# Kernel optimization log

Hardware: AMD Instinct MI355X
Metric: run time of the kernel (lower is better)

The kernel has to match this reference:

```python
import jax, jax.numpy as jnp
import numpy as np

BN_EPS = 1e-5
GRID_W = 17  # conv output width hardcoded via lat_idx*17+lon_idx

def _conv(x, w, b, stride):
    y = jax.lax.conv_general_dilated(x, w, (stride, stride), [(1, 1), (1, 1)],
                                     dimension_numbers=("NCHW", "OIHW", "NCHW"))
    return y + b[None, :, None, None]

def _bn_eval(x, g, b):
    # running_mean=0, running_var=1 (fresh BatchNorm in eval mode)
    inv = jnp.float32(1.0 / np.sqrt(1.0 + BN_EPS))
    return x * (g[None, :, None, None] * inv) + b[None, :, None, None]

def setup_inputs() -> dict:
    key = jax.random.key(0)
    ks = iter(jax.random.split(key, 64))
    def rn(shape, s=0.05):
        return jax.random.normal(next(ks), shape, jnp.float32) * s
    B, S, K = 512, 128, 64
    NR = 100000
    inp = {}
    inp["roads"] = jax.random.randint(next(ks), (B, S), 0, NR)
    inp["ratios"] = jax.random.uniform(next(ks), (B, S), jnp.float32) * 0.9 + 0.1
    inp["T"] = jax.random.normal(next(ks), (1, 1, 138, 138), jnp.float32)
    inp["lon_idx"] = jax.random.randint(next(ks), (B, K), 0, 17)
    inp["lat_idx"] = jax.random.randint(next(ks), (B, K), 0, 17)
    inp["lengths"] = jax.random.uniform(next(ks), (NR,), jnp.float32) * 100.0 + 1.0
    inp["map_u"] = jnp.arange(NR, dtype=jnp.int32)
    inp["map_s1"] = jax.random.randint(next(ks), (NR,), 0, 14)
    inp["map_s2"] = jax.random.randint(next(ks), (NR,), 0, 7)
    inp["map_s3"] = jax.random.randint(next(ks), (NR,), 0, 2)
    inp["emb_u"] = rn((NR, 128))
    inp["emb_s1"] = rn((14, 16)); inp["emb_s2"] = rn((7, 8)); inp["emb_s3"] = rn((2, 4))
    inp["rho_w1"] = rn((156, 512)); inp["rho_b1"] = jnp.zeros((512,), jnp.float32)
    inp["rho_w21"] = rn((512, 128)); inp["rho_b21"] = jnp.zeros((128,), jnp.float32)
    inp["conv1_w"] = rn((32, 1, 5, 5)); inp["conv1_b"] = jnp.zeros((32,), jnp.float32)
    inp["bn1_g"] = jnp.ones((32,), jnp.float32); inp["bn1_b"] = jnp.zeros((32,), jnp.float32)
    inp["conv2_w"] = rn((64, 32, 4, 4)); inp["conv2_b"] = jnp.zeros((64,), jnp.float32)
    inp["bn2_g"] = jnp.ones((64,), jnp.float32); inp["bn2_b"] = jnp.zeros((64,), jnp.float32)
    inp["conv3_w"] = rn((128, 64, 4, 4)); inp["conv3_b"] = jnp.zeros((128,), jnp.float32)
    inp["bn3_g"] = jnp.ones((128,), jnp.float32); inp["bn3_b"] = jnp.zeros((128,), jnp.float32)
    inp["f2_w1"] = rn((128, 256)); inp["f2_b1"] = jnp.zeros((256,), jnp.float32)
    inp["f2_w2"] = rn((256, 128)); inp["f2_b2"] = jnp.zeros((128,), jnp.float32)
    inp["f_w1"] = rn((256, 512)); inp["f_b1"] = jnp.zeros((512,), jnp.float32)
    inp["f_w21"] = rn((512, 1)); inp["f_b21"] = jnp.zeros((1,), jnp.float32)
    inp["f_w22"] = rn((512, 1)); inp["f_b22"] = jnp.zeros((1,), jnp.float32)
    return inp

def reference(roads, ratios, T, lon_idx, lat_idx, lengths, map_u, map_s1, map_s2, map_s3,
              emb_u, emb_s1, emb_s2, emb_s3, rho_w1, rho_b1, rho_w21, rho_b21,
              conv1_w, conv1_b, bn1_g, bn1_b, conv2_w, conv2_b, bn2_g, bn2_b,
              conv3_w, conv3_b, bn3_g, bn3_b, f2_w1, f2_b1, f2_w2, f2_b2,
              f_w1, f_b1, f_w21, f_b21, f_w22, f_b22):
    # road lengths / weights
    road_lens = lengths[roads] * ratios               # (B,S)
    l = road_lens.sum(axis=1)                         # (B,)
    w = road_lens / l[:, None]                        # (B,S)
    # ProbRho (eval: dropout=id, reparameterize -> mu)
    u = emb_u[map_u[roads]]                           # (B,S,128)
    s1 = emb_s1[map_s1[roads]]; s2 = emb_s2[map_s2[roads]]; s3 = emb_s3[map_s3[roads]]
    x = jnp.concatenate([u, s1, s2, s3], axis=2)      # (B,S,156)
    h = jax.nn.relu(x @ rho_w1 + rho_b1)
    rho = h @ rho_w21 + rho_b21                       # (B,S,128)
    # ProbTraffic_spatial conv stack
    t = jax.nn.leaky_relu(_bn_eval(_conv(T, conv1_w, conv1_b, 2), bn1_g, bn1_b), 0.1)
    t = jax.nn.leaky_relu(_bn_eval(_conv(t, conv2_w, conv2_b, 2), bn2_g, bn2_b), 0.1)
    t = jax.nn.leaky_relu(_bn_eval(_conv(t, conv3_w, conv3_b, 2), bn3_g, bn3_b), 0.1)  # (1,128,17,17)
    c_flat = jnp.transpose(t[0], (1, 2, 0)).reshape(-1, t.shape[1])  # (289,128)
    # fused segment gather + mean over each trajectory's grid cells
    idx = lat_idx * GRID_W + lon_idx                  # (B,K)
    c_mean = c_flat[idx].mean(axis=1)                 # (B,128)
    h2 = jax.nn.selu(c_mean @ f2_w1 + f2_b1)
    c2 = h2 @ f2_w2 + f2_b2                           # (B,128)
    # ProbTravelTime
    xcat = jnp.concatenate([rho, jnp.broadcast_to(c2[:, None, :], rho.shape)], axis=2)  # (B,S,256)
    h3 = jax.nn.relu(xcat @ f_w1 + f_b1)              # (B,S,512)
    logm = (h3 @ f_w21 + f_b21)[..., 0]               # (B,S)
    logv = (h3 @ f_w22 + f_b22)[..., 0]
    logw = jnp.log(w)
    logm_agg = jax.nn.logsumexp(logm + logw, axis=1)
    logv_agg = jax.nn.logsumexp(logv + 2.0 * logw, axis=1)
    logl = jnp.log(l)
    logmu = logl - logm_agg
    loglam = logl - 3.0 * logm_agg - logv_agg
    return (logmu, loglam)
```

## Files before the change

kernel.cpp:

```cpp
#include <hip/hip_runtime.h>
#include <math.h>

#define BB 512
#define SS 128
#define NROWS (BB*SS)
#define TMG 64
#define NBLKG (NROWS/TMG)

__device__ __forceinline__ float leaky01(float x){ return x >= 0.f ? x : 0.1f*x; }

#define BN_INV 0.9999950000374997f
#define SELU_A 1.6732632423543772f
#define SELU_S 1.0507009873554805f

typedef __attribute__((ext_vector_type(8))) short short8;
typedef __attribute__((ext_vector_type(4))) float f32x4;

__device__ __forceinline__ unsigned short f2bf(float f) {
    unsigned int u = __float_as_uint(f);
    u += 0x7fff + ((u >> 16) & 1);
    return (unsigned short)(u >> 16);
}
__device__ __forceinline__ uint2 pack4bf(float a, float b, float c, float d) {
    uint2 r;
    r.x = (unsigned int)f2bf(a) | ((unsigned int)f2bf(b) << 16);
    r.y = (unsigned int)f2bf(c) | ((unsigned int)f2bf(d) << 16);
    return r;
}

__device__ __forceinline__ unsigned short* h1p(unsigned short* base, int row, int col) {
    unsigned off = (unsigned)(row*1024 + col*2);
    off ^= (unsigned)((row & 7) << 4);
    return (unsigned short*)((char*)base + off);
}

#define PREP_N (278528 + 32768 + 131072)
#define PREP_BLOCKS (PREP_N/256)
#define CONV1_BLOCKS 578

__global__ __launch_bounds__(256) void combo1_kernel(
    const float* __restrict__ w1, const float* __restrict__ w21, const float* __restrict__ fw1,
    unsigned short* __restrict__ sw1, unsigned short* __restrict__ sw21, unsigned short* __restrict__ sw3,
    const float* __restrict__ c2w_in, const float* __restrict__ c3w_in,
    float* __restrict__ w2t, float* __restrict__ w3t,
    const float* __restrict__ T, const float* __restrict__ cw,
    const float* __restrict__ cbias, const float* __restrict__ g,
    const float* __restrict__ bb, float* __restrict__ out)
{
    if (blockIdx.x < PREP_BLOCKS) {
        int t = blockIdx.x*256 + threadIdx.x;
        if (t < 81920) {
            int j = t & 7; int r = t >> 3; int lane = r & 63; r >>= 6;
            int ks = r % 5; int nt = r / 5;
            int n = nt*16 + (lane & 15);
            int k = ks*32 + (lane >> 4)*8 + j;
            float v = (k < 156) ? w1[k*512 + n] : 0.f;
            sw1[t] = f2bf(v);
        } else if (t < 147456) {
            int u = t - 81920;
            int j = u & 7; int r = u >> 3; int lane = r & 63; r >>= 6;
            int ks = r & 15; int nt = r >> 4;
            int d = nt*16 + (lane & 15);
            int k = ks*32 + (lane >> 4)*8 + j;
            sw21[u] = f2bf(w21[k*128 + d]);
        } else if (t < 278528) {
            int u = t - 147456;
            int j = u & 7; int r = u >> 3; int lane = r & 63; r >>= 6;
            int ks = r & 7; int nt = r >> 3;
            int n = nt*16 + (lane & 15);
            int k = ks*32 + (lane >> 4)*8 + j;
            sw3[u] = f2bf(fw1[k*512 + n]);
        } else if (t < 278528 + 32768) {
            int u = t - 278528;
            int oc = u >> 9; int r = u & 511;
            int kk = r >> 5; int ic = r & 31;
            w2t[u] = c2w_in[oc*512 + ic*16 + kk];
        } else {
            int u = t - (278528 + 32768);
            int oc = u >> 10; int r = u & 1023;
            int kk = r >> 6; int ic = r & 63;
            w3t[u] = c3w_in[oc*1024 + ic*16 + kk];
        }
    } else {
        int t = (blockIdx.x - PREP_BLOCKS)*256 + threadIdx.x;
        if (t >= 32*68*68) return;
        int oc  = t & 31;
        int pos = t >> 5;
        int oy = pos / 68, ox = pos % 68;
        float acc = cbias[oc];
        #pragma unroll
        for (int ky=0; ky<5; ++ky) {
            int iy = oy*2 - 1 + ky;
            if (iy < 0 || iy >= 138) continue;
            #pragma unroll
            for (int kx=0; kx<5; ++kx) {
                int ix = ox*2 - 1 + kx;
                if (ix < 0 || ix >= 138) continue;
                acc += cw[oc*25 + ky*5 + kx] * T[iy*138 + ix];
            }
        }
        acc = acc * (g[oc]*BN_INV) + bb[oc];
        out[pos*32 + oc] = leaky01(acc);
    }
}

__global__ __launch_bounds__(256) void conv2_kernel(
    const float* __restrict__ in,
    const float* __restrict__ w2t,
    const float* __restrict__ bias, const float* __restrict__ g,
    const float* __restrict__ bb, float* __restrict__ out)
{
    int gid = blockIdx.x*256 + threadIdx.x;
    if (gid >= 64*34*34*4) return;
    int icg = gid & 3;
    int o   = gid >> 2;
    int oc  = o & 63;
    int pos = o >> 6;
    int oy = pos / 34, ox = pos % 34;
    float acc = 0.f;
    #pragma unroll
    for (int ky=0; ky<4; ++ky) {
        int iy = oy*2 - 1 + ky;
        if (iy < 0 || iy >= 68) continue;
        #pragma unroll
        for (int kx=0; kx<4; ++kx) {
            int ix = ox*2 - 1 + kx;
            if (ix < 0 || ix >= 68) continue;
            const float* ip = &in[(iy*68+ix)*32 + icg*8];
            const float* wp = &w2t[oc*512 + (ky*4+kx)*32 + icg*8];
            float4 i0 = *(const float4*)ip, i1 = *(const float4*)(ip+4);
            float4 w0 = *(const float4*)wp, w1v = *(const float4*)(wp+4);
            acc += i0.x*w0.x + i0.y*w0.y + i0.z*w0.z + i0.w*w0.w
                 + i1.x*w1v.x + i1.y*w1v.y + i1.z*w1v.z + i1.w*w1v.w;
        }
    }
    acc += __shfl_xor(acc, 1, 64);
    acc += __shfl_xor(acc, 2, 64);
    if (icg == 0) {
        acc = (acc + bias[oc]) * (g[oc]*BN_INV) + bb[oc];
        out[pos*64 + oc] = leaky01(acc);
    }
}

__global__ __launch_bounds__(256) void conv3_kernel(
    const float* __restrict__ in,
    const float* __restrict__ w3t,
    const float* __restrict__ bias, const float* __restrict__ g,
    const float* __restrict__ bb, float* __restrict__ outT)
{
    int gid = blockIdx.x*256 + threadIdx.x;
    if (gid >= 128*289*8) return;
    int icg = gid & 7;
    int o   = gid >> 3;
    int oc  = o & 127;
    int pos = o >> 7;
    int oy = pos / 17, ox = pos % 17;
    float acc = 0.f;
    #pragma unroll
    for (int ky=0; ky<4; ++ky) {
        int iy = oy*2 - 1 + ky;
        if (iy < 0 || iy >= 34) continue;
        #pragma unroll
        for (int kx=0; kx<4; ++kx) {
            int ix = ox*2 - 1 + kx;
            if (ix < 0 || ix >= 34) continue;
            const float* ip = &in[(iy*34+ix)*64 + icg*8];
            const float* wp = &w3t[oc*1024 + (ky*4+kx)*64 + icg*8];
            float4 i0 = *(const float4*)ip, i1 = *(const float4*)(ip+4);
            float4 w0 = *(const float4*)wp, w1v = *(const float4*)(wp+4);
            acc += i0.x*w0.x + i0.y*w0.y + i0.z*w0.z + i0.w*w0.w
                 + i1.x*w1v.x + i1.y*w1v.y + i1.z*w1v.z + i1.w*w1v.w;
        }
    }
    acc += __shfl_xor(acc, 1, 64);
    acc += __shfl_xor(acc, 2, 64);
    acc += __shfl_xor(acc, 4, 64);
    if (icg == 0) {
        acc = (acc + bias[oc]) * (g[oc]*BN_INV) + bb[oc];
        outT[pos*128 + oc] = leaky01(acc);
    }
}

__global__ __launch_bounds__(256) void cmh2c2_kernel(
    const float* __restrict__ t3T, const int* __restrict__ lat, const int* __restrict__ lon,
    const float* __restrict__ w1, const float* __restrict__ b1,
    const float* __restrict__ w2, const float* __restrict__ b2,
    float* __restrict__ c2b)
{
    __shared__ int   ps[64];
    __shared__ float part[256];
    __shared__ float cms[128];
    __shared__ float h2s[256];
    const int b = blockIdx.x;
    const int tid = threadIdx.x;
    if (tid < 64) ps[tid] = lat[b*64+tid]*17 + lon[b*64+tid];
    __syncthreads();
    {
        int d = tid & 127, half = tid >> 7;
        float s = 0.f;
        #pragma unroll 8
        for (int k=0; k<32; ++k) s += t3T[ps[half*32+k]*128 + d];
        part[tid] = s;
    }
    __syncthreads();
    if (tid < 128) cms[tid] = (part[tid] + part[tid+128]) * (1.f/64.f);
    __syncthreads();
    {
        float acc = b1[tid];
        #pragma unroll 8
        for (int k=0; k<128; ++k) acc += cms[k] * w1[k*256 + tid];
        h2s[tid] = acc > 0.f ? SELU_S*acc : SELU_S*SELU_A*(expf(acc)-1.f);
    }
    __syncthreads();
    {
        int d = tid & 127, half = tid >> 7;
        float acc = 0.f;
        #pragma unroll 8
        for (int k=0; k<128; ++k) acc += h2s[half*128 + k] * w2[(half*128+k)*128 + d];
        part[tid] = acc;
    }
    __syncthreads();
    if (tid < 128) c2b[b*128 + tid] = part[tid] + part[tid+128] + b2[tid];
}

#define XS_S 168
#define XC_S 264

__global__ __launch_bounds__(512, 4) void mega_kernel(
    const int* __restrict__ roads,
    const int* __restrict__ map_u, const int* __restrict__ map_s1,
    const int* __restrict__ map_s2, const int* __restrict__ map_s3,
    const float* __restrict__ emb_u, const float* __restrict__ emb_s1,
    const float* __restrict__ emb_s2, const float* __restrict__ emb_s3,
    const unsigned short* __restrict__ sw1, const float* __restrict__ b1,
    const unsigned short* __restrict__ sw21, const float* __restrict__ b21,
    const float* __restrict__ c2,
    const unsigned short* __restrict__ sw3, const float* __restrict__ fb1,
    const float* __restrict__ fw21, const float* __restrict__ fb21,
    const float* __restrict__ fw22, const float* __restrict__ fb22,
    float* __restrict__ logm, float* __restrict__ logv)
{
    __shared__ unsigned short buf[32768];
    unsigned short* xs  = buf;
    unsigned short* xcs = buf;
    float* pmv = (float*)buf;

    const int tid  = threadIdx.x;
    const int wid  = tid >> 6;
    const int lane = tid & 63;
    const int lo   = lane & 15;
    const int hi   = lane >> 4;
    const int r0   = blockIdx.x * TMG;
    const int b    = r0 >> 7;

    short8 afp[4];
    #pragma unroll
    for (int mt=0;mt<4;++mt)
        afp[mt] = *(const short8*)&sw1[((wid*4+mt)*5 + 0)*512 + lane*8];

    {
        int row = tid >> 3, seg = tid & 7;
        int road = roads[r0 + row];
        const float* src = emb_u + (long)map_u[road]*128 + seg*16;
        #pragma unroll
        for (int i=0;i<4;++i) {
            float4 v = *(const float4*)&src[i*4];
            *(uint2*)&xs[row*XS_S + seg*16 + i*4] = pack4bf(v.x, v.y, v.z, v.w);
        }
    }
    for (int idx = tid; idx < 64*32; idx += 512) {
        int row = idx >> 5, k2 = idx & 31;
        int road = roads[r0 + row];
        float v;
        if      (k2 < 16) v = emb_s1[map_s1[road]*16 + k2];
        else if (k2 < 24) v = emb_s2[map_s2[road]*8  + (k2-16)];
        else if (k2 < 28) v = emb_s3[map_s3[road]*4  + (k2-24)];
        else              v = 0.f;
        xs[row*XS_S + 128 + k2] = f2bf(v);
    }
    __syncthreads();

    short8 a2p;
    f32x4 acc1[4][4];
    {
        #pragma unroll
        for (int mt=0;mt<4;++mt)
            #pragma unroll
            for (int rg=0;rg<4;++rg) acc1[mt][rg]=(f32x4)(0.f);
        #pragma unroll
        for (int ks=0; ks<5; ++ks) {
            const int kb = ks*32 + hi*8;
            short8 bf[4];
            #pragma unroll
            for (int rg=0;rg<4;++rg)
                bf[rg] = *(const short8*)&xs[(rg*16+lo)*XS_S + kb];
            short8 af[4];
            if (ks == 0) {
                #pragma unroll
                for (int mt=0;mt<4;++mt) af[mt] = afp[mt];
            } else {
                #pragma unroll
                for (int mt=0;mt<4;++mt)
                    af[mt] = *(const short8*)&sw1[((wid*4+mt)*5 + ks)*512 + lane*8];
            }
            #pragma unroll
            for (int mt=0;mt<4;++mt)
                #pragma unroll
                for (int rg=0;rg<4;++rg)
                    acc1[mt][rg] = __builtin_amdgcn_mfma_f32_16x16x32_bf16(af[mt], bf[rg], acc1[mt][rg], 0,0,0);
        }
    }
    __syncthreads();

    {
        a2p = *(const short8*)&sw21[(wid*16 + 0)*512 + lane*8];
        const int n0 = wid * 64;
        #pragma unroll
        for (int mt=0;mt<4;++mt) {
            const int nb = n0 + mt*16 + hi*4;
            float4 bias = *(const float4*)&b1[nb];
            const float* bp = (const float*)&bias;
            #pragma unroll
            for (int rg=0;rg<4;++rg) {
                const float* a = (const float*)&acc1[mt][rg];
                float y0 = fmaxf(a[0]+bp[0], 0.f), y1 = fmaxf(a[1]+bp[1], 0.f);
                float y2 = fmaxf(a[2]+bp[2], 0.f), y3 = fmaxf(a[3]+bp[3], 0.f);
                *(uint2*)h1p(buf, rg*16+lo, nb) = pack4bf(y0,y1,y2,y3);
            }
        }
    }
    __syncthreads();

    short8 a3p[4];
    f32x4 acc2[4];
    {
        #pragma unroll
        for (int rg=0;rg<4;++rg) acc2[rg]=(f32x4)(0.f);
        #pragma unroll 4
        for (int ks=0; ks<16; ++ks) {
            const int kb = ks*32 + hi*8;
            short8 bf[4];
            #pragma unroll
            for (int rg=0;rg<4;++rg)
                bf[rg] = *(const short8*)h1p(buf, rg*16+lo, kb);
            short8 a = (ks == 0) ? a2p
                     : *(const short8*)&sw21[(wid*16 + ks)*512 + lane*8];
            #pragma unroll
            for (int rg=0;rg<4;++rg)
                acc2[rg] = __builtin_amdgcn_mfma_f32_16x16x32_bf16(a, bf[rg], acc2[rg], 0,0,0);
        }
    }
    __syncthreads();

    {
        #pragma unroll
        for (int mt=0;mt<4;++mt)
            a3p[mt] = *(const short8*)&sw3[((wid*4+mt)*8 + 0)*512 + lane*8];
        const int nb = wid*16 + hi*4;
        float4 bias = *(const float4*)&b21[nb];
        const float* bp = (const float*)&bias;
        #pragma unroll
        for (int rg=0;rg<4;++rg) {
            const float* a = (const float*)&acc2[rg];
            *(uint2*)&xcs[(rg*16+lo)*XC_S + nb] =
                pack4bf(a[0]+bp[0], a[1]+bp[1], a[2]+bp[2], a[3]+bp[3]);
        }
        int row = tid >> 3, seg = tid & 7;
        const float* src = c2 + b*128 + seg*16;
        #pragma unroll
        for (int i=0;i<4;++i) {
            float4 v = *(const float4*)&src[i*4];
            *(uint2*)&xcs[row*XC_S + 128 + seg*16 + i*4] = pack4bf(v.x, v.y, v.z, v.w);
        }
    }
    __syncthreads();

    {
        const int n0 = wid * 64;
        f32x4 acc[4][4];
        #pragma unroll
        for (int mt=0;mt<4;++mt)
            #pragma unroll
            for (int rg=0;rg<4;++rg) acc[mt][rg]=(f32x4)(0.f);
        #pragma unroll 2
        for (int ks=0; ks<8; ++ks) {
            const int kb = ks*32 + hi*8;
            short8 bf[4];
            #pragma unroll
            for (int rg=0;rg<4;++rg)
                bf[rg] = *(const short8*)&xcs[(rg*16+lo)*XC_S + kb];
            short8 af[4];
            if (ks == 0) {
                #pragma unroll
                for (int mt=0;mt<4;++mt) af[mt] = a3p[mt];
            } else {
                #pragma unroll
                for (int mt=0;mt<4;++mt)
                    af[mt] = *(const short8*)&sw3[((wid*4+mt)*8 + ks)*512 + lane*8];
            }
            #pragma unroll
            for (int mt=0;mt<4;++mt)
                #pragma unroll
                for (int rg=0;rg<4;++rg)
                    acc[mt][rg] = __builtin_amdgcn_mfma_f32_16x16x32_bf16(af[mt], bf[rg], acc[mt][rg], 0,0,0);
        }
        float sm[4] = {0.f,0.f,0.f,0.f};
        float sv[4] = {0.f,0.f,0.f,0.f};
        #pragma unroll
        for (int mt=0;mt<4;++mt) {
            const int nb = n0 + mt*16 + hi*4;
            float4 bias = *(const float4*)&fb1[nb];
            float4 wm   = *(const float4*)&fw21[nb];
            float4 wv   = *(const float4*)&fw22[nb];
            const float *bp=(const float*)&bias, *wmp=(const float*)&wm, *wvp=(const float*)&wv;
            #pragma unroll
            for (int rg=0;rg<4;++rg) {
                const float* a = (const float*)&acc[mt][rg];
                #pragma unroll
                for (int j=0;j<4;++j) {
                    float y = fmaxf(a[j]+bp[j], 0.f);
                    sm[rg] += y*wmp[j];
                    sv[rg] += y*wvp[j];
                }
            }
        }
        #pragma unroll
        for (int rg=0;rg<4;++rg) {
            sm[rg] += __shfl_xor(sm[rg], 16, 64); sm[rg] += __shfl_xor(sm[rg], 32, 64);
            sv[rg] += __shfl_xor(sv[rg], 16, 64); sv[rg] += __shfl_xor(sv[rg], 32, 64);
        }
        __syncthreads();
        if (hi == 0) {
            #pragma unroll
            for (int rg=0;rg<4;++rg) {
                pmv[wid*64 + rg*16 + lo]       = sm[rg];
                pmv[512 + wid*64 + rg*16 + lo] = sv[rg];
            }
        }
    }
    __syncthreads();
    if (tid < 64) {
        float sm = 0.f, sv = 0.f;
        #pragma unroll
        for (int w=0; w<8; ++w) {
            sm += pmv[w*64 + tid];
            sv += pmv[512 + w*64 + tid];
        }
        logm[r0+tid] = sm + fb21[0];
        logv[r0+tid] = sv + fb22[0];
    }
}

__global__ __launch_bounds__(64) void final_kernel(
    const int* __restrict__ roads, const float* __restrict__ ratios,
    const float* __restrict__ lengths,
    const float* __restrict__ logm, const float* __restrict__ logv,
    float* __restrict__ out)
{
    int b = blockIdx.x;
    int lane = threadIdx.x;
    int i0 = b*128 + lane;
    int i1 = i0 + 64;
    float rl0 = lengths[roads[i0]] * ratios[i0];
    float rl1 = lengths[roads[i1]] * ratios[i1];

    float tsum = rl0 + rl1;
    #pragma unroll
    for (int off=32; off; off>>=1) tsum += __shfl_xor(tsum, off, 64);
    float l = tsum;
    float logl = logf(l);

    float lw0 = logf(rl0) - logl;
    float lw1 = logf(rl1) - logl;

    float am0 = logm[i0] + lw0, am1 = logm[i1] + lw1;
    float av0 = logv[i0] + 2.f*lw0, av1 = logv[i1] + 2.f*lw1;

    float mm = fmaxf(am0, am1);
    #pragma unroll
    for (int off=32; off; off>>=1) mm = fmaxf(mm, __shfl_xor(mm, off, 64));
    float se = expf(am0-mm) + expf(am1-mm);
    #pragma unroll
    for (int off=32; off; off>>=1) se += __shfl_xor(se, off, 64);
    float lsem = logf(se) + mm;

    float mv = fmaxf(av0, av1);
    #pragma unroll
    for (int off=32; off; off>>=1) mv = fmaxf(mv, __shfl_xor(mv, off, 64));
    float sev = expf(av0-mv) + expf(av1-mv);
    #pragma unroll
    for (int off=32; off; off>>=1) sev += __shfl_xor(sev, off, 64);
    float lsev = logf(sev) + mv;

    if (lane == 0) {
        out[b]       = logl - lsem;
        out[512 + b] = logl - 3.f*lsem - lsev;
    }
}

extern "C" void kernel_launch(void* const* d_in, const int* in_sizes, int n_in,
                              void* d_out, int out_size, void* d_ws, size_t ws_size,
                              hipStream_t stream) {
    const int*   roads   = (const int*)  d_in[0];
    const float* ratios  = (const float*)d_in[1];
    const float* T       = (const float*)d_in[2];
    const int*   lon_idx = (const int*)  d_in[3];
    const int*   lat_idx = (const int*)  d_in[4];
    const float* lengths = (const float*)d_in[5];
    const int*   map_u   = (const int*)  d_in[6];
    const int*   map_s1  = (const int*)  d_in[7];
    const int*   map_s2  = (const int*)  d_in[8];
    const int*   map_s3  = (const int*)  d_in[9];
    const float* emb_u   = (const float*)d_in[10];
    const float* emb_s1  = (const float*)d_in[11];
    const float* emb_s2  = (const float*)d_in[12];
    const float* emb_s3  = (const float*)d_in[13];
    const float* rho_w1  = (const float*)d_in[14];
    const float* rho_b1  = (const float*)d_in[15];
    const float* rho_w21 = (const float*)d_in[16];
    const float* rho_b21 = (const float*)d_in[17];
    const float* conv1_w = (const float*)d_in[18];
    const float* conv1_b = (const float*)d_in[19];
    const float* bn1_g   = (const float*)d_in[20];
    const float* bn1_b   = (const float*)d_in[21];
    const float* conv2_w = (const float*)d_in[22];
    const float* conv2_b = (const float*)d_in[23];
    const float* bn2_g   = (const float*)d_in[24];
    const float* bn2_b   = (const float*)d_in[25];
    const float* conv3_w = (const float*)d_in[26];
    const float* conv3_b = (const float*)d_in[27];
    const float* bn3_g   = (const float*)d_in[28];
    const float* bn3_b   = (const float*)d_in[29];
    const float* f2_w1   = (const float*)d_in[30];
    const float* f2_b1   = (const float*)d_in[31];
    const float* f2_w2   = (const float*)d_in[32];
    const float* f2_b2   = (const float*)d_in[33];
    const float* f_w1    = (const float*)d_in[34];
    const float* f_b1    = (const float*)d_in[35];
    const float* f_w21   = (const float*)d_in[36];
    const float* f_b21   = (const float*)d_in[37];
    const float* f_w22   = (const float*)d_in[38];
    const float* f_b22   = (const float*)d_in[39];

    float* ws    = (float*)d_ws;
    float* t1    = ws;
    float* t2    = t1 + 147968;
    float* t3T   = t2 + 73984;
    float* c2b   = t3T + 36992;
    float* logm  = c2b + 65536;
    float* logv  = logm + 65536;
    float* w2t   = logv + 65536;
    float* w3t   = w2t + 32768;
    unsigned short* sw1  = (unsigned short*)(w3t + 131072);
    unsigned short* sw21 = sw1 + 81920;
    unsigned short* sw3  = sw21 + 65536;

    combo1_kernel<<<PREP_BLOCKS + CONV1_BLOCKS, 256, 0, stream>>>(
        rho_w1, rho_w21, f_w1, sw1, sw21, sw3,
        conv2_w, conv3_w, w2t, w3t,
        T, conv1_w, conv1_b, bn1_g, bn1_b, t1);
    conv2_kernel<<<(64*34*34*4 + 255)/256, 256, 0, stream>>>(t1, w2t, conv2_b, bn2_g, bn2_b, t2);
    conv3_kernel<<<(128*289*8 + 255)/256, 256, 0, stream>>>(t2, w3t, conv3_b, bn3_g, bn3_b, t3T);
    cmh2c2_kernel<<<512, 256, 0, stream>>>(t3T, lat_idx, lon_idx, f2_w1, f2_b1, f2_w2, f2_b2, c2b);
    mega_kernel<<<NBLKG, 512, 0, stream>>>(roads, map_u, map_s1, map_s2, map_s3,
                                           emb_u, emb_s1, emb_s2, emb_s3,
                                           sw1, rho_b1, sw21, rho_b21,
                                           c2b, sw3, f_b1, f_w21, f_b21, f_w22, f_b22,
                                           logm, logv);
    final_kernel<<<512, 64, 0, stream>>>(roads, ratios, lengths, logm, logv, (float*)d_out);
}
```

Baseline: 117.6 us.

## Process whole trajectory per block and fuse final logsumexp into mega kernel

The MLP mega kernel now handles all 128 rows of one trajectory per block with 1024 threads and 128 KB of shared memory, instead of 64 rows per block with 512 threads. Because each block owns a full trajectory, the weighted logsumexp reduction from the separate final kernel is folded in. This removes the logm/logv global round trip and one kernel launch. The warp-to-tile mapping changes so each warp covers fewer output columns over more rows, and new XOR-swizzled shared layouts replace the padded strides. The trade-off is higher register and shared-memory pressure per block, which can lower occupancy with only 512 blocks.

Measured after the change: 117.2 us. Within noise of the previous version (-0.3%).

```diff
diff --git a/kernel.cpp b/kernel.cpp
--- a/kernel.cpp
+++ b/kernel.cpp
@@ -4,7 +4,7 @@
 #define BB 512
 #define SS 128
 #define NROWS (BB*SS)
-#define TMG 64
+#define TMG 128
 #define NBLKG (NROWS/TMG)
 
 __device__ __forceinline__ float leaky01(float x){ return x >= 0.f ? x : 0.1f*x; }
@@ -28,8 +28,18 @@
     return r;
 }
 
+__device__ __forceinline__ unsigned short* xsp(unsigned short* base, int row, int col) {
+    unsigned off = (unsigned)(row*384 + col*2);
+    off ^= (unsigned)((row & 7) << 4);
+    return (unsigned short*)((char*)base + off);
+}
 __device__ __forceinline__ unsigned short* h1p(unsigned short* base, int row, int col) {
     unsigned off = (unsigned)(row*1024 + col*2);
+    off ^= (unsigned)((row & 7) << 4);
+    return (unsigned short*)((char*)base + off);
+}
+__device__ __forceinline__ unsigned short* xcp(unsigned short* base, int row, int col) {
+    unsigned off = (unsigned)(row*512 + col*2);
     off ^= (unsigned)((row & 7) << 4);
     return (unsigned short*)((char*)base + off);
 }
@@ -223,11 +233,9 @@
     if (tid < 128) c2b[b*128 + tid] = part[tid] + part[tid+128] + b2[tid];
 }
 
-#define XS_S 168
-#define XC_S 264
-
-__global__ __launch_bounds__(512, 4) void mega_kernel(
-    const int* __restrict__ roads,
+__global__ __launch_bounds__(1024, 4) void mega_kernel(
+    const int* __restrict__ roads, const float* __restrict__ ratios,
+    const float* __restrict__ lengths,
     const int* __restrict__ map_u, const int* __restrict__ map_s1,
     const int* __restrict__ map_s2, const int* __restrict__ map_s3,
     const float* __restrict__ emb_u, const float* __restrict__ emb_s1,
@@ -238,25 +246,24 @@
     const unsigned short* __restrict__ sw3, const float* __restrict__ fb1,
     const float* __restrict__ fw21, const float* __restrict__ fb21,
     const float* __restrict__ fw22, const float* __restrict__ fb22,
-    float* __restrict__ logm, float* __restrict__ logv)
+    float* __restrict__ out)
 {
-    __shared__ unsigned short buf[32768];
-    unsigned short* xs  = buf;
-    unsigned short* xcs = buf;
+    __shared__ unsigned short buf[65536];
     float* pmv = (float*)buf;
+    float* fin = (float*)buf + 4096;
 
     const int tid  = threadIdx.x;
     const int wid  = tid >> 6;
     const int lane = tid & 63;
     const int lo   = lane & 15;
     const int hi   = lane >> 4;
-    const int r0   = blockIdx.x * TMG;
-    const int b    = r0 >> 7;
-
-    short8 afp[4];
+    const int b    = blockIdx.x;
+    const int r0   = b * TMG;
+
+    short8 afp[2];
     #pragma unroll
-    for (int mt=0;mt<4;++mt)
-        afp[mt] = *(const short8*)&sw1[((wid*4+mt)*5 + 0)*512 + lane*8];
+    for (int mt=0;mt<2;++mt)
+        afp[mt] = *(const short8*)&sw1[((wid*2+mt)*5 + 0)*512 + lane*8];
 
     {
         int row = tid >> 3, seg = tid & 7;
@@ -265,10 +272,10 @@
         #pragma unroll
         for (int i=0;i<4;++i) {
             float4 v = *(const float4*)&src[i*4];
-            *(uint2*)&xs[row*XS_S + seg*16 + i*4] = pack4bf(v.x, v.y, v.z, v.w);
-        }
-    }
-    for (int idx = tid; idx < 64*32; idx += 512) {
+            *(uint2*)xsp(buf, row, seg*16 + i*4) = pack4bf(v.x, v.y, v.z, v.w);
+        }
+    }
+    for (int idx = tid; idx < 128*32; idx += 1024) {
         int row = idx >> 5, k2 = idx & 31;
         int road = roads[r0 + row];
         float v;
@@ -276,52 +283,47 @@
         else if (k2 < 24) v = emb_s2[map_s2[road]*8  + (k2-16)];
         else if (k2 < 28) v = emb_s3[map_s3[road]*4  + (k2-24)];
         else              v = 0.f;
-        xs[row*XS_S + 128 + k2] = f2bf(v);
+        *xsp(buf, row, 128 + k2) = f2bf(v);
     }
     __syncthreads();
 
     short8 a2p;
-    f32x4 acc1[4][4];
-    {
-        #pragma unroll
-        for (int mt=0;mt<4;++mt)
-            #pragma unroll
-            for (int rg=0;rg<4;++rg) acc1[mt][rg]=(f32x4)(0.f);
+    f32x4 acc1[2][8];
+    {
+        #pragma unroll
+        for (int mt=0;mt<2;++mt)
+            #pragma unroll
+            for (int rg=0;rg<8;++rg) acc1[mt][rg]=(f32x4)(0.f);
         #pragma unroll
         for (int ks=0; ks<5; ++ks) {
             const int kb = ks*32 + hi*8;
-            short8 bf[4];
-            #pragma unroll
-            for (int rg=0;rg<4;++rg)
-                bf[rg] = *(const short8*)&xs[(rg*16+lo)*XS_S + kb];
-            short8 af[4];
-            if (ks == 0) {
+            short8 af[2];
+            if (ks == 0) { af[0]=afp[0]; af[1]=afp[1]; }
+            else {
                 #pragma unroll
-                for (int mt=0;mt<4;++mt) af[mt] = afp[mt];
-            } else {
-                #pragma unroll
-                for (int mt=0;mt<4;++mt)
-                    af[mt] = *(const short8*)&sw1[((wid*4+mt)*5 + ks)*512 + lane*8];
-            }
-            #pragma unroll
-            for (int mt=0;mt<4;++mt)
-                #pragma unroll
-                for (int rg=0;rg<4;++rg)
-                    acc1[mt][rg] = __builtin_amdgcn_mfma_f32_16x16x32_bf16(af[mt], bf[rg], acc1[mt][rg], 0,0,0);
-        }
-    }
-    __syncthreads();
-
-    {
-        a2p = *(const short8*)&sw21[(wid*16 + 0)*512 + lane*8];
-        const int n0 = wid * 64;
-        #pragma unroll
-        for (int mt=0;mt<4;++mt) {
+                for (int mt=0;mt<2;++mt)
+                    af[mt] = *(const short8*)&sw1[((wid*2+mt)*5 + ks)*512 + lane*8];
+            }
+            #pragma unroll
+            for (int rg=0;rg<8;++rg) {
+                short8 bf = *(const short8*)xsp(buf, rg*16+lo, kb);
+                acc1[0][rg] = __builtin_amdgcn_mfma_f32_16x16x32_bf16(af[0], bf, acc1[0][rg], 0,0,0);
+                acc1[1][rg] = __builtin_amdgcn_mfma_f32_16x16x32_bf16(af[1], bf, acc1[1][rg], 0,0,0);
+            }
+        }
+    }
+    __syncthreads();
+
+    {
+        a2p = *(const short8*)&sw21[((wid>>1)*16 + 0)*512 + lane*8];
+        const int n0 = wid * 32;
+        #pragma unroll
+        for (int mt=0;mt<2;++mt) {
             const int nb = n0 + mt*16 + hi*4;
             float4 bias = *(const float4*)&b1[nb];
             const float* bp = (const float*)&bias;
             #pragma unroll
-            for (int rg=0;rg<4;++rg) {
+            for (int rg=0;rg<8;++rg) {
                 const float* a = (const float*)&acc1[mt][rg];
                 float y0 = fmaxf(a[0]+bp[0], 0.f), y1 = fmaxf(a[1]+bp[1], 0.f);
                 float y2 = fmaxf(a[2]+bp[2], 0.f), y3 = fmaxf(a[3]+bp[3], 0.f);
@@ -331,38 +333,38 @@
     }
     __syncthreads();
 
-    short8 a3p[4];
+    short8 a3p[2];
     f32x4 acc2[4];
-    {
-        #pragma unroll
-        for (int rg=0;rg<4;++rg) acc2[rg]=(f32x4)(0.f);
+    const int nt2 = wid >> 1;
+    const int rh  = wid & 1;
+    {
+        #pragma unroll
+        for (int i=0;i<4;++i) acc2[i]=(f32x4)(0.f);
         #pragma unroll 4
         for (int ks=0; ks<16; ++ks) {
             const int kb = ks*32 + hi*8;
-            short8 bf[4];
-            #pragma unroll
-            for (int rg=0;rg<4;++rg)
-                bf[rg] = *(const short8*)h1p(buf, rg*16+lo, kb);
             short8 a = (ks == 0) ? a2p
-                     : *(const short8*)&sw21[(wid*16 + ks)*512 + lane*8];
-            #pragma unroll
-            for (int rg=0;rg<4;++rg)
-                acc2[rg] = __builtin_amdgcn_mfma_f32_16x16x32_bf16(a, bf[rg], acc2[rg], 0,0,0);
-        }
-    }
-    __syncthreads();
-
-    {
-        #pragma unroll
-        for (int mt=0;mt<4;++mt)
-            a3p[mt] = *(const short8*)&sw3[((wid*4+mt)*8 + 0)*512 + lane*8];
-        const int nb = wid*16 + hi*4;
+                     : *(const short8*)&sw21[(nt2*16 + ks)*512 + lane*8];
+            #pragma unroll
+            for (int i=0;i<4;++i) {
+                short8 bf = *(const short8*)h1p(buf, (rh*4+i)*16+lo, kb);
+                acc2[i] = __builtin_amdgcn_mfma_f32_16x16x32_bf16(a, bf, acc2[i], 0,0,0);
+            }
+        }
+    }
+    __syncthreads();
+
+    {
+        #pragma unroll
+        for (int mt=0;mt<2;++mt)
+            a3p[mt] = *(const short8*)&sw3[((wid*2+mt)*8 + 0)*512 + lane*8];
+        const int nb = nt2*16 + hi*4;
         float4 bias = *(const float4*)&b21[nb];
         const float* bp = (const float*)&bias;
         #pragma unroll
-        for (int rg=0;rg<4;++rg) {
-            const float* a = (const float*)&acc2[rg];
-            *(uint2*)&xcs[(rg*16+lo)*XC_S + nb] =
+        for (int i=0;i<4;++i) {
+            const float* a = (const float*)&acc2[i];
+            *(uint2*)xcp(buf, (rh*4+i)*16+lo, nb) =
                 pack4bf(a[0]+bp[0], a[1]+bp[1], a[2]+bp[2], a[3]+bp[3]);
         }
         int row = tid >> 3, seg = tid & 7;
@@ -370,51 +372,47 @@
         #pragma unroll
         for (int i=0;i<4;++i) {
             float4 v = *(const float4*)&src[i*4];
-            *(uint2*)&xcs[row*XC_S + 128 + seg*16 + i*4] = pack4bf(v.x, v.y, v.z, v.w);
-        }
-    }
-    __syncthreads();
-
-    {
-        const int n0 = wid * 64;
-        f32x4 acc[4][4];
-        #pragma unroll
-        for (int mt=0;mt<4;++mt)
-            #pragma unroll
-            for (int rg=0;rg<4;++rg) acc[mt][rg]=(f32x4)(0.f);
+            *(uint2*)xcp(buf, row, 128 + seg*16 + i*4) = pack4bf(v.x, v.y, v.z, v.w);
+        }
+    }
+    __syncthreads();
+
+    float sm[8], sv[8];
+    {
+        const int n0 = wid * 32;
+        f32x4 acc[2][8];
+        #pragma unroll
+        for (int mt=0;mt<2;++mt)
+            #pragma unroll
+            for (int rg=0;rg<8;++rg) acc[mt][rg]=(f32x4)(0.f);
         #pragma unroll 2
         for (int ks=0; ks<8; ++ks) {
             const int kb = ks*32 + hi*8;
-            short8 bf[4];
-            #pragma unroll
-            for (int rg=0;rg<4;++rg)
-                bf[rg] = *(const short8*)&xcs[(rg*16+lo)*XC_S + kb];
-            short8 af[4];
-            if (ks == 0) {
+            short8 af[2];
+            if (ks == 0) { af[0]=a3p[0]; af[1]=a3p[1]; }
+            else {
                 #pragma unroll
-                for (int mt=0;mt<4;++mt) af[mt] = a3p[mt];
-            } else {
-                #pragma unroll
-                for (int mt=0;mt<4;++mt)
-                    af[mt] = *(const short8*)&sw3[((wid*4+mt)*8 + ks)*512 + lane*8];
-            }
-            #pragma unroll
-            for (int mt=0;mt<4;++mt)
-                #pragma unroll
-                for (int rg=0;rg<4;++rg)
-                    acc[mt][rg] = __builtin_amdgcn_mfma_f32_16x16x32_bf16(af[mt], bf[rg], acc[mt][rg], 0,0,0);
-        }
-        float sm[4] = {0.f,0.f,0.f,0.f};
-        float sv[4] = {0.f,0.f,0.f,0.f};
-        #pragma unroll
-        for (int mt=0;mt<4;++mt) {
+                for (int mt=0;mt<2;++mt)
+                    af[mt] = *(const short8*)&sw3[((wid*2+mt)*8 + ks)*512 + lane*8];
+            }
+            #pragma unroll
+            for (int rg=0;rg<8;++rg) {
+                short8 bf = *(const short8*)xcp(buf, rg*16+lo, kb);
+                acc[0][rg] = __builtin_amdgcn_mfma_f32_16x16x32_bf16(af[0], bf, acc[0][rg], 0,0,0);
+                acc[1][rg] = __builtin_amdgcn_mfma_f32_16x16x32_bf16(af[1], bf, acc[1][rg], 0,0,0);
+            }
+        }
+        #pragma unroll
+        for (int rg=0;rg<8;++rg){ sm[rg]=0.f; sv[rg]=0.f; }
+        #pragma unroll
+        for (int mt=0;mt<2;++mt) {
             const int nb = n0 + mt*16 + hi*4;
             float4 bias = *(const float4*)&fb1[nb];
             float4 wm   = *(const float4*)&fw21[nb];
             float4 wv   = *(const float4*)&fw22[nb];
             const float *bp=(const float*)&bias, *wmp=(const float*)&wm, *wvp=(const float*)&wv;
             #pragma unroll
-            for (int rg=0;rg<4;++rg) {
+            for (int rg=0;rg<8;++rg) {
                 const float* a = (const float*)&acc[mt][rg];
                 #pragma unroll
                 for (int j=0;j<4;++j) {
@@ -425,74 +423,66 @@
             }
         }
         #pragma unroll
-        for (int rg=0;rg<4;++rg) {
+        for (int rg=0;rg<8;++rg) {
             sm[rg] += __shfl_xor(sm[rg], 16, 64); sm[rg] += __shfl_xor(sm[rg], 32, 64);
             sv[rg] += __shfl_xor(sv[rg], 16, 64); sv[rg] += __shfl_xor(sv[rg], 32, 64);
         }
-        __syncthreads();
-        if (hi == 0) {
-            #pragma unroll
-            for (int rg=0;rg<4;++rg) {
-                pmv[wid*64 + rg*16 + lo]       = sm[rg];
-                pmv[512 + wid*64 + rg*16 + lo] = sv[rg];
-            }
-        }
-    }
-    __syncthreads();
-    if (tid < 64) {
-        float sm = 0.f, sv = 0.f;
-        #pragma unroll
-        for (int w=0; w<8; ++w) {
-            sm += pmv[w*64 + tid];
-            sv += pmv[512 + w*64 + tid];
-        }
-        logm[r0+tid] = sm + fb21[0];
-        logv[r0+tid] = sv + fb22[0];
-    }
-}
-
-__global__ __launch_bounds__(64) void final_kernel(
-    const int* __restrict__ roads, const float* __restrict__ ratios,
-    const float* __restrict__ lengths,
-    const float* __restrict__ logm, const float* __restrict__ logv,
-    float* __restrict__ out)
-{
-    int b = blockIdx.x;
-    int lane = threadIdx.x;
-    int i0 = b*128 + lane;
-    int i1 = i0 + 64;
-    float rl0 = lengths[roads[i0]] * ratios[i0];
-    float rl1 = lengths[roads[i1]] * ratios[i1];
-
-    float tsum = rl0 + rl1;
-    #pragma unroll
-    for (int off=32; off; off>>=1) tsum += __shfl_xor(tsum, off, 64);
-    float l = tsum;
-    float logl = logf(l);
-
-    float lw0 = logf(rl0) - logl;
-    float lw1 = logf(rl1) - logl;
-
-    float am0 = logm[i0] + lw0, am1 = logm[i1] + lw1;
-    float av0 = logv[i0] + 2.f*lw0, av1 = logv[i1] + 2.f*lw1;
-
-    float mm = fmaxf(am0, am1);
-    #pragma unroll
-    for (int off=32; off; off>>=1) mm = fmaxf(mm, __shfl_xor(mm, off, 64));
-    float se = expf(am0-mm) + expf(am1-mm);
-    #pragma unroll
-    for (int off=32; off; off>>=1) se += __shfl_xor(se, off, 64);
-    float lsem = logf(se) + mm;
-
-    float mv = fmaxf(av0, av1);
-    #pragma unroll
-    for (int off=32; off; off>>=1) mv = fmaxf(mv, __shfl_xor(mv, off, 64));
-    float sev = expf(av0-mv) + expf(av1-mv);
-    #pragma unroll
-    for (int off=32; off; off>>=1) sev += __shfl_xor(sev, off, 64);
-    float lsev = logf(sev) + mv;
-
-    if (lane == 0) {
+    }
+    __syncthreads();
+    if (hi == 0) {
+        #pragma unroll
+        for (int rg=0;rg<8;++rg) {
+            pmv[wid*128 + rg*16 + lo]        = sm[rg];
+            pmv[2048 + wid*128 + rg*16 + lo] = sv[rg];
+        }
+    }
+    __syncthreads();
+
+    float rl = 0.f, am = 0.f, av = 0.f;
+    if (tid < 128) {
+        float s_m = 0.f, s_v = 0.f;
+        #pragma unroll
+        for (int w=0; w<16; ++w) {
+            s_m += pmv[w*128 + tid];
+            s_v += pmv[2048 + w*128 + tid];
+        }
+        s_m += fb21[0]; s_v += fb22[0];
+        int gi = r0 + tid;
+        rl = lengths[roads[gi]] * ratios[gi];
+        float ws = rl;
+        #pragma unroll
+        for (int off=32; off; off>>=1) ws += __shfl_xor(ws, off, 64);
+        if (lane == 0) fin[wid] = ws;
+        am = s_m; av = s_v;
+    }
+    __syncthreads();
+    if (tid < 128) {
+        float l = fin[0] + fin[1];
+        float logl = logf(l);
+        float lw = logf(rl) - logl;
+        am += lw; av += 2.f*lw;
+        fin[16] = logl;
+        float mm = am, mv = av;
+        #pragma unroll
+        for (int off=32; off; off>>=1) { mm = fmaxf(mm, __shfl_xor(mm, off, 64)); mv = fmaxf(mv, __shfl_xor(mv, off, 64)); }
+        if (lane == 0) { fin[2+wid] = mm; fin[4+wid] = mv; fin[8+wid] = logl; }
+    }
+    __syncthreads();
+    if (tid < 128) {
+        float mm = fmaxf(fin[2], fin[3]);
+        float mv = fmaxf(fin[4], fin[5]);
+        float se = expf(am - mm), sev = expf(av - mv);
+        #pragma unroll
+        for (int off=32; off; off>>=1) { se += __shfl_xor(se, off, 64); sev += __shfl_xor(sev, off, 64); }
+        if (lane == 0) { fin[10+wid] = se; fin[12+wid] = sev; }
+    }
+    __syncthreads();
+    if (tid == 0) {
+        float mm = fmaxf(fin[2], fin[3]);
+        float mv = fmaxf(fin[4], fin[5]);
+        float lsem = logf(fin[10] + fin[11]) + mm;
+        float lsev = logf(fin[12] + fin[13]) + mv;
+        float logl = fin[8];
         out[b]       = logl - lsem;
         out[512 + b] = logl - 3.f*lsem - lsev;
     }
@@ -547,9 +537,7 @@
     float* t2    = t1 + 147968;
     float* t3T   = t2 + 73984;
     float* c2b   = t3T + 36992;
-    float* logm  = c2b + 65536;
-    float* logv  = logm + 65536;
-    float* w2t   = logv + 65536;
+    float* w2t   = c2b + 65536;
     float* w3t   = w2t + 32768;
     unsigned short* sw1  = (unsigned short*)(w3t + 131072);
     unsigned short* sw21 = sw1 + 81920;
@@ -562,10 +550,10 @@
     conv2_kernel<<<(64*34*34*4 + 255)/256, 256, 0, stream>>>(t1, w2t, conv2_b, bn2_g, bn2_b, t2);
     conv3_kernel<<<(128*289*8 + 255)/256, 256, 0, stream>>>(t2, w3t, conv3_b, bn3_g, bn3_b, t3T);
     cmh2c2_kernel<<<512, 256, 0, stream>>>(t3T, lat_idx, lon_idx, f2_w1, f2_b1, f2_w2, f2_b2, c2b);
-    mega_kernel<<<NBLKG, 512, 0, stream>>>(roads, map_u, map_s1, map_s2, map_s3,
-                                           emb_u, emb_s1, emb_s2, emb_s3,
-                                           sw1, rho_b1, sw21, rho_b21,
-                                           c2b, sw3, f_b1, f_w21, f_b21, f_w22, f_b22,
-                                           logm, logv);
-    final_kernel<<<512, 64, 0, stream>>>(roads, ratios, lengths, logm, logv, (float*)d_out);
-}
+    mega_kernel<<<NBLKG, 1024, 0, stream>>>(roads, ratios, lengths,
+                                            map_u, map_s1, map_s2, map_s3,
+                                            emb_u, emb_s1, emb_s2, emb_s3,
+                                            sw1, rho_b1, sw21, rho_b21,
+                                            c2b, sw3, f_b1, f_w21, f_b21, f_w22, f_b22,
+                                            (float*)d_out);
+}
```
